# Performance work log

Hardware: AMD Instinct MI355X
Metric: run time of the kernel (lower is better)

Reference implementation:

```python
import jax, jax.numpy as jnp
import numpy as np

SHIFTS = [1, 2, 4]  # matches init_kwargs 'shifts' (all in range 0 < s < channels)


def setup_inputs() -> dict:
    key = jax.random.key(0)
    k1, k2, k3 = jax.random.split(key, 3)
    B, H, L, D = 4, 1, 2048, 512
    factor = 4
    proj_in = 2 * len(SHIFTS) * D  # cli_mode='full' -> 2 components per shift
    x = jax.random.normal(k1, (B, H, L, D), dtype=jnp.float32)
    W = jax.random.normal(k2, (factor, D), dtype=jnp.float32) * 0.05
    # glorot-ish scale for the projection kernel
    proj_kernel = jax.random.normal(k3, (proj_in, D), dtype=jnp.float32) * (1.0 / np.sqrt(proj_in))
    proj_bias = jnp.zeros((D,), dtype=jnp.float32)
    return {"x": x, "W": W, "proj_kernel": proj_kernel, "proj_bias": proj_bias}


def reference(x, W, proj_kernel, proj_bias):
    # x: (B, H, L, D); W: (k, D) slot multivectors
    k, D = W.shape
    B, H, L, _ = x.shape
    # coarse[-1] treated as zeros; non-anchor slots source previous coarse vector
    coarse_prev = jnp.pad(x, ((0, 0), (0, 0), (1, 0), (0, 0)))[:, :, :-1, :]
    # src: (B, H, L, k, D) — slots 0..k-2 from coarse_prev, slot k-1 (anchor) from x
    src = jnp.concatenate(
        [jnp.repeat(coarse_prev[:, :, :, None, :], k - 1, axis=3),
         x[:, :, :, None, :]],
        axis=3,
    )
    W_b = W[None, None, None, :, :]  # (1,1,1,k,D)
    components = []
    for s in SHIFTS:
        src_s = jnp.roll(src, s, axis=-1)
        W_s_b = jnp.roll(W, s, axis=-1)[None, None, None, :, :]
        sw = src * W_s_b
        components.append(sw - W_b * src_s)        # wedge part
        components.append(jax.nn.silu(sw))          # inner part (full mode)
    g = jnp.concatenate(components, axis=-1)  # (B,H,L,k, 2*len(shifts)*D)
    fine = jnp.einsum('bhlkc,cd->bhlkd', g, proj_kernel) + proj_bias
    return fine.reshape(B, H, L * k, D)
```

## Files before the change

kernel.cpp:

```cpp
#include <hip/hip_runtime.h>
#include <cstdint>
#include <cstddef>

#define D_DIM 512
#define L_DIM 2048
#define KB_DIM 2048
#define NROWS_X 2049

typedef __bf16 bf16x8 __attribute__((ext_vector_type(8)));
typedef float  f32x4  __attribute__((ext_vector_type(4)));

__device__ __forceinline__ unsigned f2bf(float f) {
  unsigned u = __float_as_uint(f);
  u += 0x7FFF + ((u >> 16) & 1);
  return u >> 16;
}
__device__ __forceinline__ void gld_lds16(const void* g, void* l) {
  __builtin_amdgcn_global_load_lds((const __attribute__((address_space(1))) void*)g,
                                   (__attribute__((address_space(3))) void*)l,
                                   16, 0, 0);
}

__global__ void convert_x(const float* __restrict__ x, unsigned short* __restrict__ XbfZ) {
  const int b = blockIdx.y;
  const int idx = blockIdx.x * 256 + threadIdx.x;
  if (idx >= NROWS_X * 128) return;
  const int rr = idx >> 7;
  const int c4 = idx & 127;
  uint2 p = {0u, 0u};
  if (rr > 0) {
    float4 v = reinterpret_cast<const float4*>(x)[((size_t)b * L_DIM + rr - 1) * 128 + c4];
    p.x = f2bf(v.x) | (f2bf(v.y) << 16);
    p.y = f2bf(v.z) | (f2bf(v.w) << 16);
  }
  reinterpret_cast<uint2*>(XbfZ)[((size_t)b * NROWS_X + rr) * 128 + c4] = p;
}

__global__ void build_B(const float* __restrict__ P, const float* __restrict__ W,
                        unsigned short* __restrict__ Ball) {
  const int bx = blockIdx.x;
  const int j = bx >> 6, dt = (bx >> 3) & 7, ct = bx & 7;
  const int t = threadIdx.x;
  const int d = dt * 64 + (t & 63);
  const int cbase = ct * 64 + (t >> 6) * 16;
  unsigned short bufd[16];
  unsigned short bufs[3][16];
  #pragma unroll
  for (int cc = 0; cc < 16; ++cc) {
    const int c = cbase + cc;
    float qd = 0.f;
    #pragma unroll
    for (int si = 0; si < 3; ++si) {
      const int s = 1 << si;
      const int cm = (c - s) & 511, cp = (c + s) & 511;
      qd += W[j * 512 + cm] * P[((size_t)(2 * si) * 512 + c) * 512 + d]
          - W[j * 512 + cp] * P[((size_t)(2 * si) * 512 + cp) * 512 + d];
      bufs[si][cc] = (unsigned short)f2bf(P[((size_t)(2 * si + 1) * 512 + c) * 512 + d]);
    }
    bufd[cc] = (unsigned short)f2bf(qd);
  }
  unsigned short* row = Ball + (size_t)(j * 512 + d) * KB_DIM;
  *reinterpret_cast<uint4*>(&row[cbase])     = *reinterpret_cast<uint4*>(&bufd[0]);
  *reinterpret_cast<uint4*>(&row[cbase + 8]) = *reinterpret_cast<uint4*>(&bufd[8]);
  #pragma unroll
  for (int si = 0; si < 3; ++si) {
    *reinterpret_cast<uint4*>(&row[512 + si * 512 + cbase])     = *reinterpret_cast<uint4*>(&bufs[si][0]);
    *reinterpret_cast<uint4*>(&row[512 + si * 512 + cbase + 8]) = *reinterpret_cast<uint4*>(&bufs[si][8]);
  }
}

__global__ __launch_bounds__(256, 4) void gemm_main(
    const unsigned short* __restrict__ XbfZ, const unsigned short* __restrict__ Ball,
    const float* __restrict__ W, const float* __restrict__ bias,
    float* __restrict__ out) {
  __shared__ alignas(16) unsigned short Vt[2][4096];
  __shared__ alignas(16) unsigned short Btl[2][4096];
  __shared__ alignas(16) float Wr[1536];

  const int tid = threadIdx.x;
  const int bx = blockIdx.x;
  const int nt = bx >> 8;
  const int mt = bx & 255;
  const int j  = mt >> 6;
  const int b  = (mt >> 4) & 3;
  const int l0 = (mt & 15) * 128;
  const int n0 = nt * 128;

  #pragma unroll
  for (int i = 0; i < 6; ++i) {
    const int idx = tid + i * 256;
    const int si = idx >> 9, c = idx & 511;
    Wr[idx] = W[j * 512 + ((c - (1 << si)) & 511)];
  }

  const int row1   = 2 * (tid >> 3) + ((tid >> 2) & 1);
  const int chunk1 = (tid & 3) ^ ((tid >> 3) & 3);
  const unsigned short* srcV =
      XbfZ + ((size_t)b * NROWS_X + l0 + (j == 3) + row1) * 512 + chunk1 * 8;
  const unsigned short* srcB =
      Ball + ((size_t)(j * 512 + n0 + row1)) * KB_DIM + chunk1 * 8;

  const int lane = tid & 63, wv = tid >> 6;
  const int l16 = lane & 15, quad = lane >> 4;
  const int posf  = ((quad ^ ((l16 >> 1) & 3)) + 4 * (l16 & 1)) * 8;
  const int aOff0 = (wv * 16 + (l16 >> 1)) * 64 + posf;
  const int bOff0 = (l16 >> 1) * 64 + posf;
  const int wOff  = quad * 8;

  f32x4 acc[2][8];
  #pragma unroll
  for (int i = 0; i < 2; ++i)
    #pragma unroll
    for (int n = 0; n < 8; ++n)
      acc[i][n] = f32x4{0.f, 0.f, 0.f, 0.f};

  gld_lds16(srcV, &Vt[0][tid * 8]);
  gld_lds16(srcV + (size_t)64 * 512, &Vt[0][(tid + 256) * 8]);
  gld_lds16(srcB, &Btl[0][tid * 8]);
  gld_lds16(srcB + (size_t)64 * KB_DIM, &Btl[0][(tid + 256) * 8]);

  for (int it = 0; it < 64; ++it) {
    const int buf = it & 1;
    __syncthreads();
    if (it + 1 < 64) {
      const int kv = ((it + 1) * 32) & 511;
      const int kb = (it + 1) * 32;
      gld_lds16(srcV + kv, &Vt[buf ^ 1][tid * 8]);
      gld_lds16(srcV + (size_t)64 * 512 + kv, &Vt[buf ^ 1][(tid + 256) * 8]);
      gld_lds16(srcB + kb, &Btl[buf ^ 1][tid * 8]);
      gld_lds16(srcB + (size_t)64 * KB_DIM + kb, &Btl[buf ^ 1][(tid + 256) * 8]);
    }

    bf16x8 af[2];
    if (it < 16) {
      #pragma unroll
      for (int mi = 0; mi < 2; ++mi) {
        uint4 vr = *reinterpret_cast<const uint4*>(&Vt[buf][aOff0 + mi * 512]);
        af[mi] = __builtin_bit_cast(bf16x8, vr);
      }
    } else {
      const int si = (it >> 4) - 1;
      const int kwin = (it * 32) & 511;
      const float* wp = &Wr[si * 512 + kwin + wOff];
      const float4 wa = *reinterpret_cast<const float4*>(wp);
      const float4 wb = *reinterpret_cast<const float4*>(wp + 4);
      const float wreg[8] = {wa.x, wa.y, wa.z, wa.w, wb.x, wb.y, wb.z, wb.w};
      #pragma unroll
      for (int mi = 0; mi < 2; ++mi) {
        uint4 vr = *reinterpret_cast<const uint4*>(&Vt[buf][aOff0 + mi * 512]);
        unsigned vv[4] = {vr.x, vr.y, vr.z, vr.w};
        unsigned pk[4];
        #pragma unroll
        for (int e = 0; e < 4; ++e) {
          const float vlo = __uint_as_float(vv[e] << 16);
          const float vhi = __uint_as_float(vv[e] & 0xFFFF0000u);
          const float xlo = vlo * wreg[2 * e];
          const float xhi = vhi * wreg[2 * e + 1];
          const float glo = xlo * __builtin_amdgcn_rcpf(1.f + __expf(-xlo));
          const float ghi = xhi * __builtin_amdgcn_rcpf(1.f + __expf(-xhi));
          pk[e] = __builtin_amdgcn_perm(__float_as_uint(ghi) + 0x8000u,
                                        __float_as_uint(glo) + 0x8000u, 0x07060302u);
        }
        uint4 pr = {pk[0], pk[1], pk[2], pk[3]};
        af[mi] = __builtin_bit_cast(bf16x8, pr);
      }
    }

    #pragma unroll
    for (int ni = 0; ni < 8; ++ni) {
      uint4 br = *reinterpret_cast<const uint4*>(&Btl[buf][bOff0 + ni * 512]);
      bf16x8 bf = __builtin_bit_cast(bf16x8, br);
      acc[0][ni] = __builtin_amdgcn_mfma_f32_16x16x32_bf16(af[0], bf, acc[0][ni], 0, 0, 0);
      acc[1][ni] = __builtin_amdgcn_mfma_f32_16x16x32_bf16(af[1], bf, acc[1][ni], 0, 0, 0);
    }
  }

  #pragma unroll
  for (int ni = 0; ni < 8; ++ni) {
    const int d = n0 + ni * 16 + l16;
    const float bv = bias[d];
    #pragma unroll
    for (int mi = 0; mi < 2; ++mi) {
      const int lrow = l0 + wv * 32 + mi * 16 + quad * 4;
      #pragma unroll
      for (int rg = 0; rg < 4; ++rg) {
        out[((size_t)(b * L_DIM + lrow + rg) * 4 + j) * D_DIM + d] = acc[mi][ni][rg] + bv;
      }
    }
  }
}

extern "C" void kernel_launch(void* const* d_in, const int* in_sizes, int n_in,
                              void* d_out, int out_size, void* d_ws, size_t ws_size,
                              hipStream_t stream) {
  const float* x    = (const float*)d_in[0];
  const float* W    = (const float*)d_in[1];
  const float* P    = (const float*)d_in[2];
  const float* bias = (const float*)d_in[3];
  float* out = (float*)d_out;

  unsigned short* XbfZ = (unsigned short*)d_ws;
  unsigned short* Ball = XbfZ + (size_t)4 * NROWS_X * 512;

  convert_x<<<dim3(1025, 4), 256, 0, stream>>>(x, XbfZ);
  build_B<<<256, 256, 0, stream>>>(P, W, Ball);
  gemm_main<<<1024, 256, 0, stream>>>(XbfZ, Ball, W, bias, out);
}
```

Before: 208.6 us.

## Widen GEMM tile to full N, precompute SiLU A-tile once per block

The main GEMM moves from 128x128 tiles with 256 threads to 128x512 tiles with 512 threads (8 waves in a 2x4 grid), so each block covers the whole output width. The x tile is then loaded and SiLU-transformed once per block rather than once per N-tile. The SiLU/bf16 conversion is done cooperatively one stage ahead into a separate double-buffered LDS A-buffer, with a triple-buffered V ring, and the V tile is reloaded by K-window index since it repeats every 16 iterations. Blocks are mapped so each XCD handles a fixed slot j, aiming to keep that slot's B matrix in L2. The cost is more LDS per block (about 90KB), a larger accumulator footprint, and only 256 blocks, which may limit occupancy.

```diff
diff --git a/kernel.cpp b/kernel.cpp
--- a/kernel.cpp
+++ b/kernel.cpp
@@ -69,119 +69,123 @@
   }
 }
 
-__global__ __launch_bounds__(256, 4) void gemm_main(
+__global__ __launch_bounds__(512, 2) void gemm_main(
     const unsigned short* __restrict__ XbfZ, const unsigned short* __restrict__ Ball,
     const float* __restrict__ W, const float* __restrict__ bias,
     float* __restrict__ out) {
-  __shared__ alignas(16) unsigned short Vt[2][4096];
-  __shared__ alignas(16) unsigned short Btl[2][4096];
+  __shared__ alignas(16) unsigned short Vt[3][4096];
+  __shared__ alignas(16) unsigned short Btl[2][16384];
+  __shared__ alignas(16) unsigned short At[2][4096];
   __shared__ alignas(16) float Wr[1536];
 
   const int tid = threadIdx.x;
-  const int bx = blockIdx.x;
-  const int nt = bx >> 8;
-  const int mt = bx & 255;
-  const int j  = mt >> 6;
-  const int b  = (mt >> 4) & 3;
-  const int l0 = (mt & 15) * 128;
-  const int n0 = nt * 128;
-
-  #pragma unroll
-  for (int i = 0; i < 6; ++i) {
-    const int idx = tid + i * 256;
+  const int xcd = blockIdx.x & 7, slot = blockIdx.x >> 3;
+  const int j = xcd >> 1;
+  const int sub = ((xcd & 1) << 5) | slot;
+  const int b = sub >> 4;
+  const int l0 = (sub & 15) * 128;
+
+  #pragma unroll
+  for (int i = 0; i < 3; ++i) {
+    const int idx = tid + i * 512;
     const int si = idx >> 9, c = idx & 511;
     Wr[idx] = W[j * 512 + ((c - (1 << si)) & 511)];
   }
 
-  const int row1   = 2 * (tid >> 3) + ((tid >> 2) & 1);
-  const int chunk1 = (tid & 3) ^ ((tid >> 3) & 3);
+  const int row1 = 2 * (tid >> 3) + ((tid >> 2) & 1);
+  const int q1   = (tid & 3) ^ ((tid >> 3) & 3);
   const unsigned short* srcV =
-      XbfZ + ((size_t)b * NROWS_X + l0 + (j == 3) + row1) * 512 + chunk1 * 8;
+      XbfZ + ((size_t)b * NROWS_X + l0 + (j == 3) + row1) * 512 + q1 * 8;
   const unsigned short* srcB =
-      Ball + ((size_t)(j * 512 + n0 + row1)) * KB_DIM + chunk1 * 8;
+      Ball + ((size_t)j * 512 + row1) * KB_DIM + q1 * 8;
 
   const int lane = tid & 63, wv = tid >> 6;
+  const int wm = wv >> 2, wn = wv & 3;
   const int l16 = lane & 15, quad = lane >> 4;
-  const int posf  = ((quad ^ ((l16 >> 1) & 3)) + 4 * (l16 & 1)) * 8;
-  const int aOff0 = (wv * 16 + (l16 >> 1)) * 64 + posf;
-  const int bOff0 = (l16 >> 1) * 64 + posf;
-  const int wOff  = quad * 8;
-
-  f32x4 acc[2][8];
-  #pragma unroll
-  for (int i = 0; i < 2; ++i)
+  const int posf = ((quad ^ ((l16 >> 1) & 3)) + 4 * (l16 & 1)) * 8;
+  const int aOffFrag = wm * 2048 + (l16 >> 1) * 64 + posf;
+  const int bOffFrag = wn * 4096 + (l16 >> 1) * 64 + posf;
+
+  f32x4 acc[4][8];
+  #pragma unroll
+  for (int i = 0; i < 4; ++i)
     #pragma unroll
     for (int n = 0; n < 8; ++n)
       acc[i][n] = f32x4{0.f, 0.f, 0.f, 0.f};
 
-  gld_lds16(srcV, &Vt[0][tid * 8]);
-  gld_lds16(srcV + (size_t)64 * 512, &Vt[0][(tid + 256) * 8]);
-  gld_lds16(srcB, &Btl[0][tid * 8]);
-  gld_lds16(srcB + (size_t)64 * KB_DIM, &Btl[0][(tid + 256) * 8]);
-
+  gld_lds16(srcV,      &Vt[0][tid * 8]);
+  gld_lds16(srcV + 32, &Vt[1][tid * 8]);
+  #pragma unroll
+  for (int k = 0; k < 4; ++k)
+    gld_lds16(srcB + (size_t)k * 262144, &Btl[0][k * 4096 + tid * 8]);
+
+  int vA = 0, vB = 1, vC = 2;
   for (int it = 0; it < 64; ++it) {
-    const int buf = it & 1;
     __syncthreads();
-    if (it + 1 < 64) {
-      const int kv = ((it + 1) * 32) & 511;
-      const int kb = (it + 1) * 32;
-      gld_lds16(srcV + kv, &Vt[buf ^ 1][tid * 8]);
-      gld_lds16(srcV + (size_t)64 * 512 + kv, &Vt[buf ^ 1][(tid + 256) * 8]);
-      gld_lds16(srcB + kb, &Btl[buf ^ 1][tid * 8]);
-      gld_lds16(srcB + (size_t)64 * KB_DIM + kb, &Btl[buf ^ 1][(tid + 256) * 8]);
-    }
-
-    bf16x8 af[2];
-    if (it < 16) {
-      #pragma unroll
-      for (int mi = 0; mi < 2; ++mi) {
-        uint4 vr = *reinterpret_cast<const uint4*>(&Vt[buf][aOff0 + mi * 512]);
-        af[mi] = __builtin_bit_cast(bf16x8, vr);
+
+    if (it < 62)
+      gld_lds16(srcV + ((it + 2) & 15) * 32, &Vt[vC][tid * 8]);
+    if (it < 63) {
+      const int ko = (it + 1) * 32;
+      #pragma unroll
+      for (int k = 0; k < 4; ++k)
+        gld_lds16(srcB + (size_t)k * 262144 + ko,
+                  &Btl[(it + 1) & 1][k * 4096 + tid * 8]);
+    }
+
+    if (it >= 15 && it < 63) {
+      const int itn = it + 1;
+      const int si = (itn >> 4) - 1;
+      const int kwin = (itn * 32) & 511;
+      uint4 vr = *reinterpret_cast<const uint4*>(&Vt[vB][tid * 8]);
+      const float* wp = &Wr[si * 512 + kwin + q1 * 8];
+      const float4 wa4 = *reinterpret_cast<const float4*>(wp);
+      const float4 wb4 = *reinterpret_cast<const float4*>(wp + 4);
+      const float wreg[8] = {wa4.x, wa4.y, wa4.z, wa4.w, wb4.x, wb4.y, wb4.z, wb4.w};
+      unsigned vv[4] = {vr.x, vr.y, vr.z, vr.w};
+      unsigned pk[4];
+      #pragma unroll
+      for (int e = 0; e < 4; ++e) {
+        const float vlo = __uint_as_float(vv[e] << 16);
+        const float vhi = __uint_as_float(vv[e] & 0xFFFF0000u);
+        const float xlo = vlo * wreg[2 * e];
+        const float xhi = vhi * wreg[2 * e + 1];
+        const float glo = xlo * __builtin_amdgcn_rcpf(1.f + __expf(-xlo));
+        const float ghi = xhi * __builtin_amdgcn_rcpf(1.f + __expf(-xhi));
+        pk[e] = __builtin_amdgcn_perm(__float_as_uint(ghi) + 0x8000u,
+                                      __float_as_uint(glo) + 0x8000u, 0x07060302u);
       }
-    } else {
-      const int si = (it >> 4) - 1;
-      const int kwin = (it * 32) & 511;
-      const float* wp = &Wr[si * 512 + kwin + wOff];
-      const float4 wa = *reinterpret_cast<const float4*>(wp);
-      const float4 wb = *reinterpret_cast<const float4*>(wp + 4);
-      const float wreg[8] = {wa.x, wa.y, wa.z, wa.w, wb.x, wb.y, wb.z, wb.w};
-      #pragma unroll
-      for (int mi = 0; mi < 2; ++mi) {
-        uint4 vr = *reinterpret_cast<const uint4*>(&Vt[buf][aOff0 + mi * 512]);
-        unsigned vv[4] = {vr.x, vr.y, vr.z, vr.w};
-        unsigned pk[4];
-        #pragma unroll
-        for (int e = 0; e < 4; ++e) {
-          const float vlo = __uint_as_float(vv[e] << 16);
-          const float vhi = __uint_as_float(vv[e] & 0xFFFF0000u);
-          const float xlo = vlo * wreg[2 * e];
-          const float xhi = vhi * wreg[2 * e + 1];
-          const float glo = xlo * __builtin_amdgcn_rcpf(1.f + __expf(-xlo));
-          const float ghi = xhi * __builtin_amdgcn_rcpf(1.f + __expf(-xhi));
-          pk[e] = __builtin_amdgcn_perm(__float_as_uint(ghi) + 0x8000u,
-                                        __float_as_uint(glo) + 0x8000u, 0x07060302u);
-        }
-        uint4 pr = {pk[0], pk[1], pk[2], pk[3]};
-        af[mi] = __builtin_bit_cast(bf16x8, pr);
-      }
-    }
-
+      uint4 pr = {pk[0], pk[1], pk[2], pk[3]};
+      *reinterpret_cast<uint4*>(&At[itn & 1][tid * 8]) = pr;
+    }
+
+    const unsigned short* aSrc = (it < 16) ? &Vt[vA][0] : &At[it & 1][0];
+    const unsigned short* bSrc = &Btl[it & 1][0];
+    bf16x8 bfr[8];
     #pragma unroll
     for (int ni = 0; ni < 8; ++ni) {
-      uint4 br = *reinterpret_cast<const uint4*>(&Btl[buf][bOff0 + ni * 512]);
-      bf16x8 bf = __builtin_bit_cast(bf16x8, br);
-      acc[0][ni] = __builtin_amdgcn_mfma_f32_16x16x32_bf16(af[0], bf, acc[0][ni], 0, 0, 0);
-      acc[1][ni] = __builtin_amdgcn_mfma_f32_16x16x32_bf16(af[1], bf, acc[1][ni], 0, 0, 0);
-    }
+      uint4 br = *reinterpret_cast<const uint4*>(&bSrc[bOffFrag + ni * 512]);
+      bfr[ni] = __builtin_bit_cast(bf16x8, br);
+    }
+    #pragma unroll
+    for (int mi = 0; mi < 4; ++mi) {
+      uint4 ar = *reinterpret_cast<const uint4*>(&aSrc[aOffFrag + mi * 512]);
+      bf16x8 af = __builtin_bit_cast(bf16x8, ar);
+      #pragma unroll
+      for (int ni = 0; ni < 8; ++ni)
+        acc[mi][ni] = __builtin_amdgcn_mfma_f32_16x16x32_bf16(af, bfr[ni], acc[mi][ni], 0, 0, 0);
+    }
+
+    const int t = vA; vA = vB; vB = vC; vC = t;
   }
 
   #pragma unroll
   for (int ni = 0; ni < 8; ++ni) {
-    const int d = n0 + ni * 16 + l16;
+    const int d = wn * 128 + ni * 16 + l16;
     const float bv = bias[d];
     #pragma unroll
-    for (int mi = 0; mi < 2; ++mi) {
-      const int lrow = l0 + wv * 32 + mi * 16 + quad * 4;
+    for (int mi = 0; mi < 4; ++mi) {
+      const int lrow = l0 + wm * 64 + mi * 16 + quad * 4;
       #pragma unroll
       for (int rg = 0; rg < 4; ++rg) {
         out[((size_t)(b * L_DIM + lrow + rg) * 4 + j) * D_DIM + d] = acc[mi][ni][rg] + bv;
@@ -204,5 +208,5 @@
 
   convert_x<<<dim3(1025, 4), 256, 0, stream>>>(x, XbfZ);
   build_B<<<256, 256, 0, stream>>>(P, W, Ball);
-  gemm_main<<<1024, 256, 0, stream>>>(XbfZ, Ball, W, bias, out);
-}
+  gemm_main<<<256, 512, 0, stream>>>(XbfZ, Ball, W, bias, out);
+}
```

After: 199.9 us. 1.04x faster.
